# Optimization experiments

Measured on AMD Instinct MI355X. Metric: run time of the kernel, lower is better.

The kernel has to match this reference:

```python
import jax, jax.numpy as jnp
import numpy as np

B, V, T, D, H = 8, 64, 256, 256, 8
DH = D // H
LN_EPS = 1e-5


def setup_inputs() -> dict:
    key = jax.random.key(0)
    k0, k1, k2, k3 = jax.random.split(key, 4)
    x = jax.random.normal(k0, (B, V, T + 1, D), dtype=jnp.float32)
    obs_mask = jax.random.randint(k1, (B, V, T), 0, 2).astype(bool)
    ln_w = jnp.ones((D,), jnp.float32)
    ln_b = jnp.zeros((D,), jnp.float32)
    w_qkv = jax.random.normal(k2, (3 * D, D), dtype=jnp.float32) * 0.02   # torch Linear weight (out,in), no bias
    w_proj = jax.random.normal(k3, (D, D), dtype=jnp.float32) * 0.02
    b_proj = jnp.zeros((D,), jnp.float32)
    return dict(x=x, obs_mask=obs_mask, ln_w=ln_w, ln_b=ln_b,
                w_qkv=w_qkv, w_proj=w_proj, b_proj=b_proj)


def reference(x, obs_mask, ln_w, ln_b, w_qkv, w_proj, b_proj):
    b, v, t1, d = x.shape
    h, dh = H, D // H

    # LayerNorm over last dim
    mu = jnp.mean(x, axis=-1, keepdims=True)
    var = jnp.mean(jnp.square(x - mu), axis=-1, keepdims=True)
    xn = (x - mu) * jax.lax.rsqrt(var + LN_EPS) * ln_w + ln_b

    # QKV projection: (B,V,T1,3D) -> (B,V,T1,3,H,dh)
    qkv = jnp.einsum('bvtd,ed->bvte', xn, w_qkv).reshape(b, v, t1, 3, h, dh)
    qf = qkv[:, :, :, 0]  # (B,V,T1,H,dh)
    kf = qkv[:, :, :, 1]
    vf = qkv[:, :, :, 2]

    # Queries from position 0 only: (B,H,V,dh)
    q = jnp.transpose(qf[:, :, 0], (0, 2, 1, 3))

    # Keys: masked mean over time (query token at pos 0 always observed)
    mask = jnp.concatenate([jnp.ones((b, v, 1), bool), obs_mask], axis=2)  # (B,V,T1)
    mf = mask[..., None, None].astype(kf.dtype)                            # (B,V,T1,1,1)
    cnt = jnp.clip(mask.sum(axis=2).astype(kf.dtype), 1.0)[:, :, None, None]
    k = (kf * mf).sum(axis=2) / cnt                                        # (B,V,H,dh)
    k = jnp.transpose(k, (0, 2, 1, 3))                                     # (B,H,V,dh)

    # Small cross-variable attention matrix (B,H,V,V)
    scale = dh ** -0.5
    attn = jax.nn.softmax(jnp.einsum('bhqd,bhkd->bhqk', q, k) * scale, axis=-1)

    # Values packed with temporal structure: (B,H,V,dh,T1)
    vp = jnp.transpose(vf, (0, 3, 1, 4, 2))
    out = jnp.einsum('bhqk,bhkdt->bhqdt', attn, vp)                        # (B,H,V,dh,T1)

    # Unpack back to (B,V,T1,D)
    out = jnp.transpose(out, (0, 2, 4, 1, 3)).reshape(b, v, t1, d)
    out = out @ w_proj.T + b_proj
    return x + out
```

## Files before the change

kernel.cpp:

```cpp
#include <hip/hip_runtime.h>
#include <hip/hip_bf16.h>

typedef unsigned short u16;
typedef __attribute__((ext_vector_type(8))) short short8;
typedef __attribute__((ext_vector_type(4))) float f32x4;

#define B_ 8
#define V_ 64
#define T_ 256
#define T1_ 257
#define D_ 256
#define H_ 8
#define DH_ 32

__device__ __forceinline__ u16 f2bf(float f){
  union { float f; unsigned int u; } v; v.f = f;
  unsigned int u = v.u;
  return (u16)((u + 0x7fffu + ((u >> 16) & 1u)) >> 16);
}

__global__ void k1_ln(const float* __restrict__ x, const int* __restrict__ mask,
                      const float* __restrict__ lnw, const float* __restrict__ lnb,
                      const float* __restrict__ wqkv, const float* __restrict__ wproj,
                      float* __restrict__ musig, float* __restrict__ xsum,
                      u16* __restrict__ wv, u16* __restrict__ wp){
  if (blockIdx.x >= 512){
    int j = (blockIdx.x - 512) * 512 + threadIdx.x;
    wv[j] = f2bf(wqkv[131072 + j]);
    wp[j] = f2bf(wproj[j]);
    return;
  }
  int bv = blockIdx.x;
  int tid = threadIdx.x;
  int lane = tid & 63, wid = tid >> 6;
  int half = lane >> 5, l32 = lane & 31;
  int c8 = l32 * 8;
  __shared__ float xsred[8][512];
  float4 w0 = *(const float4*)&lnw[c8], w1 = *(const float4*)&lnw[c8 + 4];
  float4 b0 = *(const float4*)&lnb[c8], b1 = *(const float4*)&lnb[c8 + 4];
  float xs[8];
  #pragma unroll
  for (int j = 0; j < 8; ++j) xs[j] = 0.f;
  for (int p = wid; p < 129; p += 8){
    int t = p * 2 + half;
    bool valid = (t < T1_);
    float4 a0 = {0.f,0.f,0.f,0.f}, a1 = {0.f,0.f,0.f,0.f};
    if (valid){
      const float* gp = &x[((long)bv * T1_ + t) * D_ + c8];
      a0 = *(const float4*)gp; a1 = *(const float4*)(gp + 4);
    }
    float s  = a0.x + a0.y + a0.z + a0.w + a1.x + a1.y + a1.z + a1.w;
    float s2 = a0.x*a0.x + a0.y*a0.y + a0.z*a0.z + a0.w*a0.w
             + a1.x*a1.x + a1.y*a1.y + a1.z*a1.z + a1.w*a1.w;
    #pragma unroll
    for (int off = 1; off < 32; off <<= 1){
      s  += __shfl_xor(s,  off, 64);
      s2 += __shfl_xor(s2, off, 64);
    }
    float mu   = s * (1.f / 256.f);
    float var  = s2 * (1.f / 256.f) - mu * mu;
    float rstd = rsqrtf(var + 1e-5f);
    if (valid){
      if (l32 == 0){
        musig[((long)bv * T1_ + t) * 2]     = mu;
        musig[((long)bv * T1_ + t) * 2 + 1] = rstd;
      }
      int m = (t == 0) ? 1 : mask[bv * T_ + (t - 1)];
      if (m){
        xs[0] += (a0.x - mu) * rstd * w0.x + b0.x;
        xs[1] += (a0.y - mu) * rstd * w0.y + b0.y;
        xs[2] += (a0.z - mu) * rstd * w0.z + b0.z;
        xs[3] += (a0.w - mu) * rstd * w0.w + b0.w;
        xs[4] += (a1.x - mu) * rstd * w1.x + b1.x;
        xs[5] += (a1.y - mu) * rstd * w1.y + b1.y;
        xs[6] += (a1.z - mu) * rstd * w1.z + b1.z;
        xs[7] += (a1.w - mu) * rstd * w1.w + b1.w;
      }
    }
  }
  #pragma unroll
  for (int j = 0; j < 8; ++j) xsred[wid][half * 256 + c8 + j] = xs[j];
  __syncthreads();
  if (tid < 256){
    float r = 0.f;
    #pragma unroll
    for (int w2 = 0; w2 < 8; ++w2) r += xsred[w2][tid] + xsred[w2][256 + tid];
    xsum[bv * D_ + tid] = r;
  }
}

__global__ void k2a_qk(const float* __restrict__ x, const int* __restrict__ mask,
                       const float* __restrict__ lnw, const float* __restrict__ lnb,
                       const float* __restrict__ wqkv,
                       const float* __restrict__ musig, const float* __restrict__ xsum,
                       float* __restrict__ qout, float* __restrict__ kout){
  int bv = blockIdx.x, tid = threadIdx.x;
  int lane = tid & 63, wid = tid >> 6;
  __shared__ __align__(16) float xn0[D_];
  __shared__ __align__(16) float xs[D_];
  __shared__ float redc[4];
  int s = mask[bv * T_ + tid];
  #pragma unroll
  for (int off = 32; off >= 1; off >>= 1) s += __shfl_down(s, off, 64);
  if (lane == 0) redc[wid] = (float)s;
  __syncthreads();
  float cnt = 1.f + redc[0] + redc[1] + redc[2] + redc[3];
  float mu = musig[((long)bv * T1_) * 2], rstd = musig[((long)bv * T1_) * 2 + 1];
  xn0[tid] = (x[((long)bv * T1_) * D_ + tid] - mu) * rstd * lnw[tid] + lnb[tid];
  xs[tid]  = xsum[bv * D_ + tid] * (1.f / cnt);
  __syncthreads();
  float4 xq = *(const float4*)&xn0[lane * 4];
  float4 xk = *(const float4*)&xs[lane * 4];
  int e0 = (blockIdx.y * 4 + wid) * 16;
  for (int i = 0; i < 16; ++i){
    int e = e0 + i;
    float4 wq4 = *(const float4*)&wqkv[(long)e * D_ + lane * 4];
    float4 wk4 = *(const float4*)&wqkv[(long)(256 + e) * D_ + lane * 4];
    float sq = xq.x*wq4.x + xq.y*wq4.y + xq.z*wq4.z + xq.w*wq4.w;
    float sk = xk.x*wk4.x + xk.y*wk4.y + xk.z*wk4.z + xk.w*wk4.w;
    #pragma unroll
    for (int off = 32; off >= 1; off >>= 1){
      sq += __shfl_down(sq, off, 64);
      sk += __shfl_down(sk, off, 64);
    }
    if (lane == 0){ qout[bv * D_ + e] = sq; kout[bv * D_ + e] = sk; }
  }
}

__global__ void k2b_attn(const float* __restrict__ q, const float* __restrict__ k,
                         u16* __restrict__ attn){
  int bh = blockIdx.x; int b = bh >> 3, h = bh & 7;
  int tid = threadIdx.x;
  int lane = tid & 63, wid = tid >> 6;
  __shared__ float qs[64][33], ks[64][33];
  #pragma unroll
  for (int j = 0; j < 2; ++j){
    int i4 = tid * 2 + j;
    int r = i4 >> 3, c4 = (i4 & 7) * 4;
    float4 vq = *(const float4*)&q[((long)(b * V_ + r)) * D_ + h * DH_ + c4];
    float4 vk = *(const float4*)&k[((long)(b * V_ + r)) * D_ + h * DH_ + c4];
    qs[r][c4] = vq.x; qs[r][c4+1] = vq.y; qs[r][c4+2] = vq.z; qs[r][c4+3] = vq.w;
    ks[r][c4] = vk.x; ks[r][c4+1] = vk.y; ks[r][c4+2] = vk.z; ks[r][c4+3] = vk.w;
  }
  __syncthreads();
  const float scale = 0.17677669529663687f;
  for (int i = blockIdx.y * 4; i < blockIdx.y * 4 + 4; ++i){
    int qr = i * 4 + wid;
    float a = 0.f;
    #pragma unroll
    for (int d = 0; d < DH_; ++d) a += qs[qr][d] * ks[lane][d];
    a *= scale;
    float mx = a;
    #pragma unroll
    for (int off = 1; off < 64; off <<= 1) mx = fmaxf(mx, __shfl_xor(mx, off, 64));
    float e = __expf(a - mx);
    float sum = e;
    #pragma unroll
    for (int off = 1; off < 64; off <<= 1) sum += __shfl_xor(sum, off, 64);
    attn[((long)bh * 64 + qr) * 64 + lane] = f2bf(e * (1.f / sum));
  }
}

__global__ __launch_bounds__(512, 4) void k3_main(
    const float* __restrict__ x, const float* __restrict__ lnw, const float* __restrict__ lnb,
    const float* __restrict__ bproj, const float* __restrict__ musig,
    const u16* __restrict__ wv, const u16* __restrict__ wp,
    const u16* __restrict__ attn, float* __restrict__ out){
  constexpr int XS = 264;
  constexpr int TSL = 64 * XS;
  __shared__ __align__(16) u16 Xs[2 * TSL];
  __shared__ float lnw_s[D_], lnb_s[D_], bp_s[D_];
  __shared__ float ms_s[2][V_][2];

  int bt = blockIdx.x; int b = bt / 129, ty = bt % 129;
  int t0 = ty * 2;
  int tid = threadIdx.x;
  int w = tid >> 6, lane = tid & 63, lm = lane & 15, lq = lane >> 4;
  int cw = w * 32;
  int h = w;

  if (tid < 256){ lnw_s[tid] = lnw[tid]; lnb_s[tid] = lnb[tid]; bp_s[tid] = bproj[tid]; }
  else {
    int i = tid - 256;
    int tslot = i >> 7, vr = (i >> 1) & 63, sel = i & 1;
    int t = t0 + tslot; if (t > 256) t = 256;
    ms_s[tslot][vr][sel] = musig[(((long)b * V_ + vr) * T1_ + t) * 2 + sel];
  }
  __syncthreads();

  #pragma unroll
  for (int i = 0; i < 8; ++i){
    int seg = i * 512 + tid;
    int vr2 = seg >> 5;
    int tslot = vr2 >> 6, vr = vr2 & 63;
    int c8 = (seg & 31) * 8;
    int t = t0 + tslot;
    float4 a0 = {0.f,0.f,0.f,0.f}, a1 = {0.f,0.f,0.f,0.f};
    if (t < T1_){
      const float* gp = x + (((long)b * V_ + vr) * T1_ + t) * D_ + c8;
      a0 = *(const float4*)gp;
      a1 = *(const float4*)(gp + 4);
    }
    float mu = ms_s[tslot][vr][0], rs = ms_s[tslot][vr][1];
    float av[8] = {a0.x, a0.y, a0.z, a0.w, a1.x, a1.y, a1.z, a1.w};
    union { u16 us[8]; uint4 q4; } pk;
    #pragma unroll
    for (int j = 0; j < 8; ++j)
      pk.us[j] = f2bf((av[j] - mu) * rs * lnw_s[c8 + j] + lnb_s[c8 + j]);
    *(uint4*)&Xs[tslot * TSL + vr * XS + c8] = pk.q4;
  }
  __syncthreads();

  f32x4 acc1[2][4][2];
  #pragma unroll
  for (int tt = 0; tt < 2; ++tt)
    #pragma unroll
    for (int mt = 0; mt < 4; ++mt)
      #pragma unroll
      for (int nt = 0; nt < 2; ++nt) acc1[tt][mt][nt] = (f32x4){0.f, 0.f, 0.f, 0.f};
  for (int kk = 0; kk < 8; ++kk){
    short8 bfr[2];
    #pragma unroll
    for (int nt = 0; nt < 2; ++nt)
      bfr[nt] = *(const short8*)&wv[(long)(cw + nt * 16 + lm) * D_ + kk * 32 + lq * 8];
    #pragma unroll
    for (int tt = 0; tt < 2; ++tt){
      short8 af[4];
      #pragma unroll
      for (int mt = 0; mt < 4; ++mt)
        af[mt] = *(const short8*)&Xs[tt * TSL + (mt * 16 + lm) * XS + kk * 32 + lq * 8];
      #pragma unroll
      for (int mt = 0; mt < 4; ++mt)
        #pragma unroll
        for (int nt = 0; nt < 2; ++nt)
          acc1[tt][mt][nt] = __builtin_amdgcn_mfma_f32_16x16x32_bf16(af[mt], bfr[nt], acc1[tt][mt][nt], 0, 0, 0);
    }
  }
  unsigned int pw[2][4][2][2];
  #pragma unroll
  for (int tt = 0; tt < 2; ++tt)
    #pragma unroll
    for (int mt = 0; mt < 4; ++mt)
      #pragma unroll
      for (int nt = 0; nt < 2; ++nt)
        #pragma unroll
        for (int p = 0; p < 2; ++p)
          pw[tt][mt][nt][p] = (unsigned int)f2bf(acc1[tt][mt][nt][2*p])
                            | ((unsigned int)f2bf(acc1[tt][mt][nt][2*p+1]) << 16);
  __syncthreads();

  u16* vtw = &Xs[w * 4224];
  #pragma unroll
  for (int tt = 0; tt < 2; ++tt)
    #pragma unroll
    for (int mt = 0; mt < 4; ++mt)
      #pragma unroll
      for (int nt = 0; nt < 2; ++nt){
        int c  = nt * 16 + lm;
        int v8 = mt * 2 + (lq >> 1);
        int off = tt * 2048 + c * 64 + ((v8 ^ (lm & 7)) * 8) + (lq & 1) * 4;
        union { unsigned int wq[2]; uint2 q2; } pv;
        pv.wq[0] = pw[tt][mt][nt][0]; pv.wq[1] = pw[tt][mt][nt][1];
        *(uint2*)&vtw[off] = pv.q2;
      }

  short8 atf[2][4];
  #pragma unroll
  for (int kk = 0; kk < 2; ++kk)
    #pragma unroll
    for (int mt = 0; mt < 4; ++mt)
      atf[kk][mt] = *(const short8*)&attn[((long)(b * H_ + h) * 64 + mt * 16 + lm) * 64 + kk * 32 + lq * 8];
  f32x4 acc2[2][4][2];
  #pragma unroll
  for (int tt = 0; tt < 2; ++tt)
    #pragma unroll
    for (int mt = 0; mt < 4; ++mt)
      #pragma unroll
      for (int nt = 0; nt < 2; ++nt) acc2[tt][mt][nt] = (f32x4){0.f, 0.f, 0.f, 0.f};
  #pragma unroll
  for (int kk = 0; kk < 2; ++kk)
    #pragma unroll
    for (int tt = 0; tt < 2; ++tt){
      short8 bfr[2];
      #pragma unroll
      for (int nt = 0; nt < 2; ++nt){
        int c = nt * 16 + lm;
        int v8 = kk * 4 + lq;
        bfr[nt] = *(const short8*)&vtw[tt * 2048 + c * 64 + ((v8 ^ (lm & 7)) * 8)];
      }
      #pragma unroll
      for (int mt = 0; mt < 4; ++mt)
        #pragma unroll
        for (int nt = 0; nt < 2; ++nt)
          acc2[tt][mt][nt] = __builtin_amdgcn_mfma_f32_16x16x32_bf16(atf[kk][mt], bfr[nt], acc2[tt][mt][nt], 0, 0, 0);
    }
  __syncthreads();

  #pragma unroll
  for (int tt = 0; tt < 2; ++tt)
    #pragma unroll
    for (int mt = 0; mt < 4; ++mt)
      #pragma unroll
      for (int nt = 0; nt < 2; ++nt){
        int col = h * 32 + nt * 16 + lm;
        #pragma unroll
        for (int r = 0; r < 4; ++r){
          int row = mt * 16 + lq * 4 + r;
          Xs[tt * TSL + row * XS + col] = f2bf(acc2[tt][mt][nt][r]);
        }
      }
  __syncthreads();

  f32x4 acc3[2][4][2];
  #pragma unroll
  for (int tt = 0; tt < 2; ++tt)
    #pragma unroll
    for (int mt = 0; mt < 4; ++mt)
      #pragma unroll
      for (int nt = 0; nt < 2; ++nt) acc3[tt][mt][nt] = (f32x4){0.f, 0.f, 0.f, 0.f};
  for (int kk = 0; kk < 8; ++kk){
    short8 bfr[2];
    #pragma unroll
    for (int nt = 0; nt < 2; ++nt)
      bfr[nt] = *(const short8*)&wp[(long)(cw + nt * 16 + lm) * D_ + kk * 32 + lq * 8];
    #pragma unroll
    for (int tt = 0; tt < 2; ++tt){
      short8 af[4];
      #pragma unroll
      for (int mt = 0; mt < 4; ++mt)
        af[mt] = *(const short8*)&Xs[tt * TSL + (mt * 16 + lm) * XS + kk * 32 + lq * 8];
      #pragma unroll
      for (int mt = 0; mt < 4; ++mt)
        #pragma unroll
        for (int nt = 0; nt < 2; ++nt)
          acc3[tt][mt][nt] = __builtin_amdgcn_mfma_f32_16x16x32_bf16(af[mt], bfr[nt], acc3[tt][mt][nt], 0, 0, 0);
    }
  }
  #pragma unroll
  for (int tt = 0; tt < 2; ++tt){
    int t = t0 + tt;
    if (t < T1_){
      #pragma unroll
      for (int mt = 0; mt < 4; ++mt)
        #pragma unroll
        for (int nt = 0; nt < 2; ++nt){
          int e = cw + nt * 16 + lm;
          #pragma unroll
          for (int r = 0; r < 4; ++r){
            int vr = mt * 16 + lq * 4 + r;
            long g = (((long)b * V_ + vr) * T1_ + t) * D_ + e;
            out[g] = acc3[tt][mt][nt][r] + bp_s[e] + x[g];
          }
        }
    }
  }
}

extern "C" void kernel_launch(void* const* d_in, const int* in_sizes, int n_in,
                              void* d_out, int out_size, void* d_ws, size_t ws_size,
                              hipStream_t stream){
  const float* x     = (const float*)d_in[0];
  const int*   mask  = (const int*)d_in[1];
  const float* lnw   = (const float*)d_in[2];
  const float* lnb   = (const float*)d_in[3];
  const float* wqkv  = (const float*)d_in[4];
  const float* wproj = (const float*)d_in[5];
  const float* bproj = (const float*)d_in[6];
  float* out = (float*)d_out;
  char* ws = (char*)d_ws;
  float* musig = (float*)(ws);
  float* xsum  = (float*)(ws + 1052672);
  float* qbuf  = (float*)(ws + 1576960);
  float* kbuf  = (float*)(ws + 2101248);
  u16*   attn  = (u16*)  (ws + 2625536);
  u16*   wv    = (u16*)  (ws + 3149824);
  u16*   wp    = (u16*)  (ws + 3280896);

  k1_ln<<<640, 512, 0, stream>>>(x, mask, lnw, lnb, wqkv, wproj, musig, xsum, wv, wp);
  k2a_qk<<<dim3(512, 4), 256, 0, stream>>>(x, mask, lnw, lnb, wqkv, musig, xsum, qbuf, kbuf);
  k2b_attn<<<dim3(64, 4), 256, 0, stream>>>(qbuf, kbuf, attn);
  k3_main<<<B_ * 129, 512, 0, stream>>>(x, lnw, lnb, bproj, musig, wv, wp, attn, out);
}
```

Measured before the change: 391.6 us.

## Make main kernel persistent with double-buffered prefetch of next tile

```diff
diff --git a/kernel.cpp b/kernel.cpp
--- a/kernel.cpp
+++ b/kernel.cpp
@@ -19,29 +19,29 @@
   return (u16)((u + 0x7fffu + ((u >> 16) & 1u)) >> 16);
 }
 
+__global__ void k0_conv(const float* __restrict__ wqkv, const float* __restrict__ wproj,
+                        u16* __restrict__ wv, u16* __restrict__ wp, float* __restrict__ xsum){
+  int i = blockIdx.x * 256 + threadIdx.x;
+  if (i < 65536) wv[i] = f2bf(wqkv[131072 + i]);
+  else           wp[i - 65536] = f2bf(wproj[i - 65536]);
+  xsum[i] = 0.f;
+}
+
 __global__ void k1_ln(const float* __restrict__ x, const int* __restrict__ mask,
                       const float* __restrict__ lnw, const float* __restrict__ lnb,
-                      const float* __restrict__ wqkv, const float* __restrict__ wproj,
-                      float* __restrict__ musig, float* __restrict__ xsum,
-                      u16* __restrict__ wv, u16* __restrict__ wp){
-  if (blockIdx.x >= 512){
-    int j = (blockIdx.x - 512) * 512 + threadIdx.x;
-    wv[j] = f2bf(wqkv[131072 + j]);
-    wp[j] = f2bf(wproj[j]);
-    return;
-  }
+                      float* __restrict__ musig, float* __restrict__ xsum){
   int bv = blockIdx.x;
   int tid = threadIdx.x;
   int lane = tid & 63, wid = tid >> 6;
   int half = lane >> 5, l32 = lane & 31;
   int c8 = l32 * 8;
-  __shared__ float xsred[8][512];
+  __shared__ float xsred[4][512];
   float4 w0 = *(const float4*)&lnw[c8], w1 = *(const float4*)&lnw[c8 + 4];
   float4 b0 = *(const float4*)&lnb[c8], b1 = *(const float4*)&lnb[c8 + 4];
   float xs[8];
   #pragma unroll
   for (int j = 0; j < 8; ++j) xs[j] = 0.f;
-  for (int p = wid; p < 129; p += 8){
+  for (int p = blockIdx.y * 4 + wid; p < 129; p += 16){
     int t = p * 2 + half;
     bool valid = (t < T1_);
     float4 a0 = {0.f,0.f,0.f,0.f}, a1 = {0.f,0.f,0.f,0.f};
@@ -81,12 +81,10 @@
   #pragma unroll
   for (int j = 0; j < 8; ++j) xsred[wid][half * 256 + c8 + j] = xs[j];
   __syncthreads();
-  if (tid < 256){
-    float r = 0.f;
-    #pragma unroll
-    for (int w2 = 0; w2 < 8; ++w2) r += xsred[w2][tid] + xsred[w2][256 + tid];
-    xsum[bv * D_ + tid] = r;
-  }
+  float r = xsred[0][tid] + xsred[1][tid] + xsred[2][tid] + xsred[3][tid]
+          + xsred[0][256 + tid] + xsred[1][256 + tid] + xsred[2][256 + tid] + xsred[3][256 + tid];
+  if (tid < 256) atomicAdd(&xsum[bv * D_ + tid], r);
+  else           atomicAdd(&xsum[bv * D_ + tid - 256], 0.f);
 }
 
 __global__ void k2a_qk(const float* __restrict__ x, const int* __restrict__ mask,
@@ -144,7 +142,7 @@
   }
   __syncthreads();
   const float scale = 0.17677669529663687f;
-  for (int i = blockIdx.y * 4; i < blockIdx.y * 4 + 4; ++i){
+  for (int i = 0; i < 16; ++i){
     int qr = i * 4 + wid;
     float a = 0.f;
     #pragma unroll
@@ -161,48 +159,59 @@
   }
 }
 
-__global__ __launch_bounds__(512, 4) void k3_main(
+__global__ __launch_bounds__(512, 2) void k3_main(
     const float* __restrict__ x, const float* __restrict__ lnw, const float* __restrict__ lnb,
     const float* __restrict__ bproj, const float* __restrict__ musig,
     const u16* __restrict__ wv, const u16* __restrict__ wp,
     const u16* __restrict__ attn, float* __restrict__ out){
   constexpr int XS = 264;
   constexpr int TSL = 64 * XS;
-  __shared__ __align__(16) u16 Xs[2 * TSL];
+  constexpr int PBUF = 2 * TSL;
+  __shared__ __align__(16) u16 Xs[2 * PBUF];
   __shared__ float lnw_s[D_], lnb_s[D_], bp_s[D_];
-  __shared__ float ms_s[2][V_][2];
-
-  int bt = blockIdx.x; int b = bt / 129, ty = bt % 129;
-  int t0 = ty * 2;
+
+  int g = blockIdx.x;
   int tid = threadIdx.x;
   int w = tid >> 6, lane = tid & 63, lm = lane & 15, lq = lane >> 4;
   int cw = w * 32;
   int h = w;
+  int c8 = (tid & 31) * 8;
+  int vrow = tid >> 5;
 
   if (tid < 256){ lnw_s[tid] = lnw[tid]; lnb_s[tid] = lnb[tid]; bp_s[tid] = bproj[tid]; }
-  else {
-    int i = tid - 256;
-    int tslot = i >> 7, vr = (i >> 1) & 63, sel = i & 1;
-    int t = t0 + tslot; if (t > 256) t = 256;
-    ms_s[tslot][vr][sel] = musig[(((long)b * V_ + vr) * T1_ + t) * 2 + sel];
-  }
-  __syncthreads();
-
+
+  int nP = (g < 8) ? 5 : 4;
+
+  float4 xa[8][2];
+  float2 msv[8];
+
+  {
+    int P = g; int bb = P / 129, ty = P % 129, t0n = ty * 2;
+    #pragma unroll
+    for (int ii = 0; ii < 8; ++ii){
+      int vr2 = ii * 16 + vrow;
+      int tslot = vr2 >> 6, vr = vr2 & 63;
+      int t = t0n + tslot;
+      if (t < T1_){
+        const float* gp = x + (((long)bb * V_ + vr) * T1_ + t) * D_ + c8;
+        xa[ii][0] = *(const float4*)gp;
+        xa[ii][1] = *(const float4*)(gp + 4);
+        msv[ii] = *(const float2*)&musig[(((long)bb * V_ + vr) * T1_ + t) * 2];
+      } else {
+        xa[ii][0] = (float4){0.f,0.f,0.f,0.f};
+        xa[ii][1] = (float4){0.f,0.f,0.f,0.f};
+        msv[ii] = (float2){0.f, 1.f};
+      }
+    }
+  }
+  __syncthreads();
   #pragma unroll
-  for (int i = 0; i < 8; ++i){
-    int seg = i * 512 + tid;
-    int vr2 = seg >> 5;
+  for (int ii = 0; ii < 8; ++ii){
+    int vr2 = ii * 16 + vrow;
     int tslot = vr2 >> 6, vr = vr2 & 63;
-    int c8 = (seg & 31) * 8;
-    int t = t0 + tslot;
-    float4 a0 = {0.f,0.f,0.f,0.f}, a1 = {0.f,0.f,0.f,0.f};
-    if (t < T1_){
-      const float* gp = x + (((long)b * V_ + vr) * T1_ + t) * D_ + c8;
-      a0 = *(const float4*)gp;
-      a1 = *(const float4*)(gp + 4);
-    }
-    float mu = ms_s[tslot][vr][0], rs = ms_s[tslot][vr][1];
-    float av[8] = {a0.x, a0.y, a0.z, a0.w, a1.x, a1.y, a1.z, a1.w};
+    float mu = msv[ii].x, rs = msv[ii].y;
+    float av[8] = {xa[ii][0].x, xa[ii][0].y, xa[ii][0].z, xa[ii][0].w,
+                   xa[ii][1].x, xa[ii][1].y, xa[ii][1].z, xa[ii][1].w};
     union { u16 us[8]; uint4 q4; } pk;
     #pragma unroll
     for (int j = 0; j < 8; ++j)
@@ -211,148 +220,197 @@
   }
   __syncthreads();
 
-  f32x4 acc1[2][4][2];
-  #pragma unroll
-  for (int tt = 0; tt < 2; ++tt)
-    #pragma unroll
-    for (int mt = 0; mt < 4; ++mt)
-      #pragma unroll
-      for (int nt = 0; nt < 2; ++nt) acc1[tt][mt][nt] = (f32x4){0.f, 0.f, 0.f, 0.f};
-  for (int kk = 0; kk < 8; ++kk){
-    short8 bfr[2];
-    #pragma unroll
-    for (int nt = 0; nt < 2; ++nt)
-      bfr[nt] = *(const short8*)&wv[(long)(cw + nt * 16 + lm) * D_ + kk * 32 + lq * 8];
-    #pragma unroll
-    for (int tt = 0; tt < 2; ++tt){
-      short8 af[4];
-      #pragma unroll
-      for (int mt = 0; mt < 4; ++mt)
-        af[mt] = *(const short8*)&Xs[tt * TSL + (mt * 16 + lm) * XS + kk * 32 + lq * 8];
+  for (int p = 0; p < nP; ++p){
+    u16* buf  = &Xs[(p & 1) * PBUF];
+    u16* nbuf = &Xs[((p + 1) & 1) * PBUF];
+    int P = g + p * 256;
+    int b = P / 129, ty = P % 129, t0 = ty * 2;
+    bool pf = (p + 1 < nP);
+
+    f32x4 acc1[2][4][2];
+    #pragma unroll
+    for (int tt = 0; tt < 2; ++tt)
+      #pragma unroll
+      for (int mt = 0; mt < 4; ++mt)
+        #pragma unroll
+        for (int nt = 0; nt < 2; ++nt) acc1[tt][mt][nt] = (f32x4){0.f, 0.f, 0.f, 0.f};
+    for (int kk = 0; kk < 8; ++kk){
+      short8 bfr[2];
+      #pragma unroll
+      for (int nt = 0; nt < 2; ++nt)
+        bfr[nt] = *(const short8*)&wv[(long)(cw + nt * 16 + lm) * D_ + kk * 32 + lq * 8];
+      #pragma unroll
+      for (int tt = 0; tt < 2; ++tt){
+        short8 af[4];
+        #pragma unroll
+        for (int mt = 0; mt < 4; ++mt)
+          af[mt] = *(const short8*)&buf[tt * TSL + (mt * 16 + lm) * XS + kk * 32 + lq * 8];
+        #pragma unroll
+        for (int mt = 0; mt < 4; ++mt)
+          #pragma unroll
+          for (int nt = 0; nt < 2; ++nt)
+            acc1[tt][mt][nt] = __builtin_amdgcn_mfma_f32_16x16x32_bf16(af[mt], bfr[nt], acc1[tt][mt][nt], 0, 0, 0);
+      }
+    }
+
+    short8 atf[2][4];
+    #pragma unroll
+    for (int kk = 0; kk < 2; ++kk)
+      #pragma unroll
+      for (int mt = 0; mt < 4; ++mt)
+        atf[kk][mt] = *(const short8*)&attn[((long)(b * H_ + h) * 64 + mt * 16 + lm) * 64 + kk * 32 + lq * 8];
+    __builtin_amdgcn_sched_barrier(0);
+    if (pf){
+      int Pn = g + (p + 1) * 256;
+      int bb = Pn / 129, tyn = Pn % 129, t0n = tyn * 2;
+      #pragma unroll
+      for (int ii = 0; ii < 8; ++ii){
+        int vr2 = ii * 16 + vrow;
+        int tslot = vr2 >> 6, vr = vr2 & 63;
+        int t = t0n + tslot;
+        if (t < T1_){
+          const float* gp = x + (((long)bb * V_ + vr) * T1_ + t) * D_ + c8;
+          xa[ii][0] = *(const float4*)gp;
+          xa[ii][1] = *(const float4*)(gp + 4);
+          msv[ii] = *(const float2*)&musig[(((long)bb * V_ + vr) * T1_ + t) * 2];
+        } else {
+          xa[ii][0] = (float4){0.f,0.f,0.f,0.f};
+          xa[ii][1] = (float4){0.f,0.f,0.f,0.f};
+          msv[ii] = (float2){0.f, 1.f};
+        }
+      }
+    }
+
+    unsigned int pw[2][4][2][2];
+    #pragma unroll
+    for (int tt = 0; tt < 2; ++tt)
       #pragma unroll
       for (int mt = 0; mt < 4; ++mt)
         #pragma unroll
         for (int nt = 0; nt < 2; ++nt)
-          acc1[tt][mt][nt] = __builtin_amdgcn_mfma_f32_16x16x32_bf16(af[mt], bfr[nt], acc1[tt][mt][nt], 0, 0, 0);
-    }
-  }
-  unsigned int pw[2][4][2][2];
-  #pragma unroll
-  for (int tt = 0; tt < 2; ++tt)
-    #pragma unroll
-    for (int mt = 0; mt < 4; ++mt)
-      #pragma unroll
-      for (int nt = 0; nt < 2; ++nt)
-        #pragma unroll
-        for (int p = 0; p < 2; ++p)
-          pw[tt][mt][nt][p] = (unsigned int)f2bf(acc1[tt][mt][nt][2*p])
-                            | ((unsigned int)f2bf(acc1[tt][mt][nt][2*p+1]) << 16);
-  __syncthreads();
-
-  u16* vtw = &Xs[w * 4224];
-  #pragma unroll
-  for (int tt = 0; tt < 2; ++tt)
-    #pragma unroll
-    for (int mt = 0; mt < 4; ++mt)
-      #pragma unroll
-      for (int nt = 0; nt < 2; ++nt){
-        int c  = nt * 16 + lm;
-        int v8 = mt * 2 + (lq >> 1);
-        int off = tt * 2048 + c * 64 + ((v8 ^ (lm & 7)) * 8) + (lq & 1) * 4;
-        union { unsigned int wq[2]; uint2 q2; } pv;
-        pv.wq[0] = pw[tt][mt][nt][0]; pv.wq[1] = pw[tt][mt][nt][1];
-        *(uint2*)&vtw[off] = pv.q2;
-      }
-
-  short8 atf[2][4];
-  #pragma unroll
-  for (int kk = 0; kk < 2; ++kk)
-    #pragma unroll
-    for (int mt = 0; mt < 4; ++mt)
-      atf[kk][mt] = *(const short8*)&attn[((long)(b * H_ + h) * 64 + mt * 16 + lm) * 64 + kk * 32 + lq * 8];
-  f32x4 acc2[2][4][2];
-  #pragma unroll
-  for (int tt = 0; tt < 2; ++tt)
-    #pragma unroll
-    for (int mt = 0; mt < 4; ++mt)
-      #pragma unroll
-      for (int nt = 0; nt < 2; ++nt) acc2[tt][mt][nt] = (f32x4){0.f, 0.f, 0.f, 0.f};
-  #pragma unroll
-  for (int kk = 0; kk < 2; ++kk)
-    #pragma unroll
-    for (int tt = 0; tt < 2; ++tt){
-      short8 bfr[2];
-      #pragma unroll
-      for (int nt = 0; nt < 2; ++nt){
-        int c = nt * 16 + lm;
-        int v8 = kk * 4 + lq;
-        bfr[nt] = *(const short8*)&vtw[tt * 2048 + c * 64 + ((v8 ^ (lm & 7)) * 8)];
-      }
-      #pragma unroll
-      for (int mt = 0; mt < 4; ++mt)
-        #pragma unroll
-        for (int nt = 0; nt < 2; ++nt)
-          acc2[tt][mt][nt] = __builtin_amdgcn_mfma_f32_16x16x32_bf16(atf[kk][mt], bfr[nt], acc2[tt][mt][nt], 0, 0, 0);
-    }
-  __syncthreads();
-
-  #pragma unroll
-  for (int tt = 0; tt < 2; ++tt)
-    #pragma unroll
-    for (int mt = 0; mt < 4; ++mt)
-      #pragma unroll
-      for (int nt = 0; nt < 2; ++nt){
-        int col = h * 32 + nt * 16 + lm;
-        #pragma unroll
-        for (int r = 0; r < 4; ++r){
-          int row = mt * 16 + lq * 4 + r;
-          Xs[tt * TSL + row * XS + col] = f2bf(acc2[tt][mt][nt][r]);
+          #pragma unroll
+          for (int q = 0; q < 2; ++q)
+            pw[tt][mt][nt][q] = (unsigned int)f2bf(acc1[tt][mt][nt][2*q])
+                              | ((unsigned int)f2bf(acc1[tt][mt][nt][2*q+1]) << 16);
+    __syncthreads();
+
+    u16* vtw = &buf[w * 4224];
+    #pragma unroll
+    for (int tt = 0; tt < 2; ++tt)
+      #pragma unroll
+      for (int mt = 0; mt < 4; ++mt)
+        #pragma unroll
+        for (int nt = 0; nt < 2; ++nt){
+          int c  = nt * 16 + lm;
+          int v8 = mt * 2 + (lq >> 1);
+          int off = tt * 2048 + c * 64 + ((v8 ^ (lm & 7)) * 8) + (lq & 1) * 4;
+          union { unsigned int wq[2]; uint2 q2; } pv;
+          pv.wq[0] = pw[tt][mt][nt][0]; pv.wq[1] = pw[tt][mt][nt][1];
+          *(uint2*)&vtw[off] = pv.q2;
         }
-      }
-  __syncthreads();
-
-  f32x4 acc3[2][4][2];
-  #pragma unroll
-  for (int tt = 0; tt < 2; ++tt)
-    #pragma unroll
-    for (int mt = 0; mt < 4; ++mt)
-      #pragma unroll
-      for (int nt = 0; nt < 2; ++nt) acc3[tt][mt][nt] = (f32x4){0.f, 0.f, 0.f, 0.f};
-  for (int kk = 0; kk < 8; ++kk){
-    short8 bfr[2];
-    #pragma unroll
-    for (int nt = 0; nt < 2; ++nt)
-      bfr[nt] = *(const short8*)&wp[(long)(cw + nt * 16 + lm) * D_ + kk * 32 + lq * 8];
-    #pragma unroll
-    for (int tt = 0; tt < 2; ++tt){
-      short8 af[4];
-      #pragma unroll
-      for (int mt = 0; mt < 4; ++mt)
-        af[mt] = *(const short8*)&Xs[tt * TSL + (mt * 16 + lm) * XS + kk * 32 + lq * 8];
-      #pragma unroll
-      for (int mt = 0; mt < 4; ++mt)
-        #pragma unroll
-        for (int nt = 0; nt < 2; ++nt)
-          acc3[tt][mt][nt] = __builtin_amdgcn_mfma_f32_16x16x32_bf16(af[mt], bfr[nt], acc3[tt][mt][nt], 0, 0, 0);
-    }
-  }
-  #pragma unroll
-  for (int tt = 0; tt < 2; ++tt){
-    int t = t0 + tt;
-    if (t < T1_){
-      #pragma unroll
-      for (int mt = 0; mt < 4; ++mt)
+
+    f32x4 acc2[2][4][2];
+    #pragma unroll
+    for (int tt = 0; tt < 2; ++tt)
+      #pragma unroll
+      for (int mt = 0; mt < 4; ++mt)
+        #pragma unroll
+        for (int nt = 0; nt < 2; ++nt) acc2[tt][mt][nt] = (f32x4){0.f, 0.f, 0.f, 0.f};
+    #pragma unroll
+    for (int kk = 0; kk < 2; ++kk)
+      #pragma unroll
+      for (int tt = 0; tt < 2; ++tt){
+        short8 bfr[2];
         #pragma unroll
         for (int nt = 0; nt < 2; ++nt){
-          int e = cw + nt * 16 + lm;
+          int c = nt * 16 + lm;
+          int v8 = kk * 4 + lq;
+          bfr[nt] = *(const short8*)&vtw[tt * 2048 + c * 64 + ((v8 ^ (lm & 7)) * 8)];
+        }
+        #pragma unroll
+        for (int mt = 0; mt < 4; ++mt)
+          #pragma unroll
+          for (int nt = 0; nt < 2; ++nt)
+            acc2[tt][mt][nt] = __builtin_amdgcn_mfma_f32_16x16x32_bf16(atf[kk][mt], bfr[nt], acc2[tt][mt][nt], 0, 0, 0);
+      }
+    __syncthreads();
+
+    #pragma unroll
+    for (int tt = 0; tt < 2; ++tt)
+      #pragma unroll
+      for (int mt = 0; mt < 4; ++mt)
+        #pragma unroll
+        for (int nt = 0; nt < 2; ++nt){
+          int col = h * 32 + nt * 16 + lm;
           #pragma unroll
           for (int r = 0; r < 4; ++r){
-            int vr = mt * 16 + lq * 4 + r;
-            long g = (((long)b * V_ + vr) * T1_ + t) * D_ + e;
-            out[g] = acc3[tt][mt][nt][r] + bp_s[e] + x[g];
+            int row = mt * 16 + lq * 4 + r;
+            buf[tt * TSL + row * XS + col] = f2bf(acc2[tt][mt][nt][r]);
           }
         }
-    }
+    __syncthreads();
+
+    f32x4 acc3[2][4][2];
+    #pragma unroll
+    for (int tt = 0; tt < 2; ++tt)
+      #pragma unroll
+      for (int mt = 0; mt < 4; ++mt)
+        #pragma unroll
+        for (int nt = 0; nt < 2; ++nt) acc3[tt][mt][nt] = (f32x4){0.f, 0.f, 0.f, 0.f};
+    for (int kk = 0; kk < 8; ++kk){
+      short8 bfr[2];
+      #pragma unroll
+      for (int nt = 0; nt < 2; ++nt)
+        bfr[nt] = *(const short8*)&wp[(long)(cw + nt * 16 + lm) * D_ + kk * 32 + lq * 8];
+      #pragma unroll
+      for (int tt = 0; tt < 2; ++tt){
+        short8 af[4];
+        #pragma unroll
+        for (int mt = 0; mt < 4; ++mt)
+          af[mt] = *(const short8*)&buf[tt * TSL + (mt * 16 + lm) * XS + kk * 32 + lq * 8];
+        #pragma unroll
+        for (int mt = 0; mt < 4; ++mt)
+          #pragma unroll
+          for (int nt = 0; nt < 2; ++nt)
+            acc3[tt][mt][nt] = __builtin_amdgcn_mfma_f32_16x16x32_bf16(af[mt], bfr[nt], acc3[tt][mt][nt], 0, 0, 0);
+      }
+    }
+
+    if (pf){
+      #pragma unroll
+      for (int ii = 0; ii < 8; ++ii){
+        int vr2 = ii * 16 + vrow;
+        int tslot = vr2 >> 6, vr = vr2 & 63;
+        float mu = msv[ii].x, rs = msv[ii].y;
+        float av[8] = {xa[ii][0].x, xa[ii][0].y, xa[ii][0].z, xa[ii][0].w,
+                       xa[ii][1].x, xa[ii][1].y, xa[ii][1].z, xa[ii][1].w};
+        union { u16 us[8]; uint4 q4; } pk;
+        #pragma unroll
+        for (int j = 0; j < 8; ++j)
+          pk.us[j] = f2bf((av[j] - mu) * rs * lnw_s[c8 + j] + lnb_s[c8 + j]);
+        *(uint4*)&nbuf[tslot * TSL + vr * XS + c8] = pk.q4;
+      }
+    }
+
+    #pragma unroll
+    for (int tt = 0; tt < 2; ++tt){
+      int t = t0 + tt;
+      if (t < T1_){
+        #pragma unroll
+        for (int mt = 0; mt < 4; ++mt)
+          #pragma unroll
+          for (int nt = 0; nt < 2; ++nt){
+            int e = cw + nt * 16 + lm;
+            #pragma unroll
+            for (int r = 0; r < 4; ++r){
+              int vr = mt * 16 + lq * 4 + r;
+              long gidx = (((long)b * V_ + vr) * T1_ + t) * D_ + e;
+              out[gidx] = acc3[tt][mt][nt][r] + bp_s[e] + x[gidx];
+            }
+          }
+      }
+    }
+    __syncthreads();
   }
 }
 
@@ -376,8 +434,9 @@
   u16*   wv    = (u16*)  (ws + 3149824);
   u16*   wp    = (u16*)  (ws + 3280896);
 
-  k1_ln<<<640, 512, 0, stream>>>(x, mask, lnw, lnb, wqkv, wproj, musig, xsum, wv, wp);
+  k0_conv<<<512, 256, 0, stream>>>(wqkv, wproj, wv, wp, xsum);
+  k1_ln<<<dim3(512, 4), 256, 0, stream>>>(x, mask, lnw, lnb, musig, xsum);
   k2a_qk<<<dim3(512, 4), 256, 0, stream>>>(x, mask, lnw, lnb, wqkv, musig, xsum, qbuf, kbuf);
-  k2b_attn<<<dim3(64, 4), 256, 0, stream>>>(qbuf, kbuf, attn);
-  k3_main<<<B_ * 129, 512, 0, stream>>>(x, lnw, lnb, bproj, musig, wv, wp, attn, out);
-}
+  k2b_attn<<<64, 256, 0, stream>>>(qbuf, kbuf, attn);
+  k3_main<<<256, 512, 0, stream>>>(x, lnw, lnb, bproj, musig, wv, wp, attn, out);
+}
```

Measured after the change: 493.8 us. +26.1%, slower.

## Fuse Q/K projection into LayerNorm kernel and collapse attention grid

Applied to the files above, without the earlier changes.

```diff
diff --git a/kernel.cpp b/kernel.cpp
--- a/kernel.cpp
+++ b/kernel.cpp
@@ -19,11 +19,11 @@
   return (u16)((u + 0x7fffu + ((u >> 16) & 1u)) >> 16);
 }
 
-__global__ void k1_ln(const float* __restrict__ x, const int* __restrict__ mask,
-                      const float* __restrict__ lnw, const float* __restrict__ lnb,
-                      const float* __restrict__ wqkv, const float* __restrict__ wproj,
-                      float* __restrict__ musig, float* __restrict__ xsum,
-                      u16* __restrict__ wv, u16* __restrict__ wp){
+__global__ void k1_fused(const float* __restrict__ x, const int* __restrict__ mask,
+                         const float* __restrict__ lnw, const float* __restrict__ lnb,
+                         const float* __restrict__ wqkv, const float* __restrict__ wproj,
+                         float* __restrict__ musig, float* __restrict__ qout,
+                         float* __restrict__ kout, u16* __restrict__ wv, u16* __restrict__ wp){
   if (blockIdx.x >= 512){
     int j = (blockIdx.x - 512) * 512 + threadIdx.x;
     wv[j] = f2bf(wqkv[131072 + j]);
@@ -36,6 +36,10 @@
   int half = lane >> 5, l32 = lane & 31;
   int c8 = l32 * 8;
   __shared__ float xsred[8][512];
+  __shared__ float redc[8];
+  __shared__ float ms0[2];
+  __shared__ __align__(16) float xn0s[D_];
+  __shared__ __align__(16) float xsv[D_];
   float4 w0 = *(const float4*)&lnw[c8], w1 = *(const float4*)&lnw[c8 + 4];
   float4 b0 = *(const float4*)&lnb[c8], b1 = *(const float4*)&lnb[c8 + 4];
   float xs[8];
@@ -64,6 +68,7 @@
       if (l32 == 0){
         musig[((long)bv * T1_ + t) * 2]     = mu;
         musig[((long)bv * T1_ + t) * 2 + 1] = rstd;
+        if (t == 0){ ms0[0] = mu; ms0[1] = rstd; }
       }
       int m = (t == 0) ? 1 : mask[bv * T_ + (t - 1)];
       if (m){
@@ -80,50 +85,44 @@
   }
   #pragma unroll
   for (int j = 0; j < 8; ++j) xsred[wid][half * 256 + c8 + j] = xs[j];
+  int sm = (tid < 256) ? mask[bv * T_ + tid] : 0;
+  #pragma unroll
+  for (int off = 32; off >= 1; off >>= 1) sm += __shfl_down(sm, off, 64);
+  if (lane == 0) redc[wid] = (float)sm;
   __syncthreads();
   if (tid < 256){
     float r = 0.f;
     #pragma unroll
     for (int w2 = 0; w2 < 8; ++w2) r += xsred[w2][tid] + xsred[w2][256 + tid];
-    xsum[bv * D_ + tid] = r;
-  }
-}
-
-__global__ void k2a_qk(const float* __restrict__ x, const int* __restrict__ mask,
-                       const float* __restrict__ lnw, const float* __restrict__ lnb,
-                       const float* __restrict__ wqkv,
-                       const float* __restrict__ musig, const float* __restrict__ xsum,
-                       float* __restrict__ qout, float* __restrict__ kout){
-  int bv = blockIdx.x, tid = threadIdx.x;
-  int lane = tid & 63, wid = tid >> 6;
-  __shared__ __align__(16) float xn0[D_];
-  __shared__ __align__(16) float xs[D_];
-  __shared__ float redc[4];
-  int s = mask[bv * T_ + tid];
-  #pragma unroll
-  for (int off = 32; off >= 1; off >>= 1) s += __shfl_down(s, off, 64);
-  if (lane == 0) redc[wid] = (float)s;
-  __syncthreads();
-  float cnt = 1.f + redc[0] + redc[1] + redc[2] + redc[3];
-  float mu = musig[((long)bv * T1_) * 2], rstd = musig[((long)bv * T1_) * 2 + 1];
-  xn0[tid] = (x[((long)bv * T1_) * D_ + tid] - mu) * rstd * lnw[tid] + lnb[tid];
-  xs[tid]  = xsum[bv * D_ + tid] * (1.f / cnt);
-  __syncthreads();
-  float4 xq = *(const float4*)&xn0[lane * 4];
-  float4 xk = *(const float4*)&xs[lane * 4];
-  int e0 = (blockIdx.y * 4 + wid) * 16;
+    xsv[tid] = r;
+    xn0s[tid] = (x[((long)bv * T1_) * D_ + tid] - ms0[0]) * ms0[1] * lnw[tid] + lnb[tid];
+  }
+  __syncthreads();
+  float cnt = 1.f + redc[0] + redc[1] + redc[2] + redc[3]
+                  + redc[4] + redc[5] + redc[6] + redc[7];
+  float invc = 1.f / cnt;
+  int hw = tid >> 5;
+  float4 xq0 = *(const float4*)&xn0s[c8], xq1 = *(const float4*)&xn0s[c8 + 4];
+  float4 xk0 = *(const float4*)&xsv[c8],  xk1 = *(const float4*)&xsv[c8 + 4];
   for (int i = 0; i < 16; ++i){
-    int e = e0 + i;
-    float4 wq4 = *(const float4*)&wqkv[(long)e * D_ + lane * 4];
-    float4 wk4 = *(const float4*)&wqkv[(long)(256 + e) * D_ + lane * 4];
-    float sq = xq.x*wq4.x + xq.y*wq4.y + xq.z*wq4.z + xq.w*wq4.w;
-    float sk = xk.x*wk4.x + xk.y*wk4.y + xk.z*wk4.z + xk.w*wk4.w;
-    #pragma unroll
-    for (int off = 32; off >= 1; off >>= 1){
-      sq += __shfl_down(sq, off, 64);
-      sk += __shfl_down(sk, off, 64);
-    }
-    if (lane == 0){ qout[bv * D_ + e] = sq; kout[bv * D_ + e] = sk; }
+    int e = hw * 16 + i;
+    const float* wq = &wqkv[(long)e * D_ + c8];
+    const float* wk = &wqkv[(long)(256 + e) * D_ + c8];
+    float4 q0 = *(const float4*)wq, q1 = *(const float4*)(wq + 4);
+    float4 k0 = *(const float4*)wk, k1 = *(const float4*)(wk + 4);
+    float sq = xq0.x*q0.x + xq0.y*q0.y + xq0.z*q0.z + xq0.w*q0.w
+             + xq1.x*q1.x + xq1.y*q1.y + xq1.z*q1.z + xq1.w*q1.w;
+    float sk = xk0.x*k0.x + xk0.y*k0.y + xk0.z*k0.z + xk0.w*k0.w
+             + xk1.x*k1.x + xk1.y*k1.y + xk1.z*k1.z + xk1.w*k1.w;
+    #pragma unroll
+    for (int off = 1; off < 32; off <<= 1){
+      sq += __shfl_xor(sq, off, 64);
+      sk += __shfl_xor(sk, off, 64);
+    }
+    if (l32 == 0){
+      qout[bv * D_ + e] = sq;
+      kout[bv * D_ + e] = sk * invc;
+    }
   }
 }
 
@@ -144,7 +143,7 @@
   }
   __syncthreads();
   const float scale = 0.17677669529663687f;
-  for (int i = blockIdx.y * 4; i < blockIdx.y * 4 + 4; ++i){
+  for (int i = 0; i < 16; ++i){
     int qr = i * 4 + wid;
     float a = 0.f;
     #pragma unroll
@@ -369,15 +368,13 @@
   float* out = (float*)d_out;
   char* ws = (char*)d_ws;
   float* musig = (float*)(ws);
-  float* xsum  = (float*)(ws + 1052672);
   float* qbuf  = (float*)(ws + 1576960);
   float* kbuf  = (float*)(ws + 2101248);
   u16*   attn  = (u16*)  (ws + 2625536);
   u16*   wv    = (u16*)  (ws + 3149824);
   u16*   wp    = (u16*)  (ws + 3280896);
 
-  k1_ln<<<640, 512, 0, stream>>>(x, mask, lnw, lnb, wqkv, wproj, musig, xsum, wv, wp);
-  k2a_qk<<<dim3(512, 4), 256, 0, stream>>>(x, mask, lnw, lnb, wqkv, musig, xsum, qbuf, kbuf);
-  k2b_attn<<<dim3(64, 4), 256, 0, stream>>>(qbuf, kbuf, attn);
+  k1_fused<<<640, 512, 0, stream>>>(x, mask, lnw, lnb, wqkv, wproj, musig, qbuf, kbuf, wv, wp);
+  k2b_attn<<<64, 256, 0, stream>>>(qbuf, kbuf, attn);
   k3_main<<<B_ * 129, 512, 0, stream>>>(x, lnw, lnb, bproj, musig, wv, wp, attn, out);
 }
```

Result: no change. 389.1 us (-0.6%).
